# Optimization experiments

Hardware: AMD Instinct MI355X
Metric: run time of the kernel (lower is better)

The kernel has to match this reference:

```python
import jax, jax.numpy as jnp
import numpy as np

B, N, D = 8, 4096, 256
E = 32768
H, C = 4, 64  # heads, per-head dim (hid_dim=256 // heads=4)
NEG_SLOPE = 0.2


def layernorm(x, g, b, eps=1e-5):
    m = jnp.mean(x, axis=-1, keepdims=True)
    v = jnp.var(x, axis=-1, keepdims=True)
    return (x - m) * jax.lax.rsqrt(v + eps) * g + b


def setup_inputs() -> dict:
    key = jax.random.key(0)
    ks = jax.random.split(key, 12)
    def glorot(k, shape):
        lim = np.sqrt(6.0 / (shape[-2] + shape[-1]))
        return jax.random.uniform(k, shape, jnp.float32, -lim, lim)
    return {
        "x": jax.random.normal(ks[0], (B, N, D), jnp.float32),
        "edge_index": jax.random.randint(ks[1], (2, E), 0, N, jnp.int32),
        "W_K": glorot(ks[2], (H * C, D)), "b_K": jnp.zeros((H * C,), jnp.float32),
        "W_V": glorot(ks[3], (H * C, D)), "b_V": jnp.zeros((H * C,), jnp.float32),
        "att_r": glorot(ks[4], (1, H, C)),
        "ln0_g": jnp.ones((H * C,), jnp.float32), "ln0_b": jnp.zeros((H * C,), jnp.float32),
        "ln1_g": jnp.ones((H * C,), jnp.float32), "ln1_b": jnp.zeros((H * C,), jnp.float32),
        "W1": glorot(ks[5], (H * C, H * C)), "b1": jnp.zeros((H * C,), jnp.float32),
        "W2": glorot(ks[6], (H * C, H * C)), "b2": jnp.zeros((H * C,), jnp.float32),
    }


def reference(x, edge_index, W_K, b_K, W_V, b_V, att_r, ln0_g, ln0_b, ln1_g, ln1_b, W1, b1, W2, b2):
    Bq, Nq = x.shape[0], x.shape[1]
    S = Nq  # number of destination segments (fixed for jit)
    src, dst = edge_index[0], edge_index[1]
    # projections -> [B, N, H, C]
    xK = (jnp.einsum('bnd,hd->bnh', x, W_K) + b_K).reshape(Bq, Nq, H, C)
    xV = (jnp.einsum('bnd,hd->bnh', x, W_V) + b_V).reshape(Bq, Nq, H, C)
    # per-node attention logits [B, N, H]
    alpha = jnp.sum(xK * att_r[None], axis=-1)
    # gather to edges, leaky-relu, segment softmax over dst
    a = alpha[:, src]  # [B, E, H]
    a = jnp.where(a >= 0, a, NEG_SLOPE * a)
    a_t = jnp.transpose(a, (1, 0, 2))  # [E, B, H]
    seg_max = jax.ops.segment_max(a_t, dst, num_segments=S)
    seg_max = jnp.where(jnp.isfinite(seg_max), seg_max, 0.0)
    ex = jnp.exp(a_t - seg_max[dst])
    den = jax.ops.segment_sum(ex, dst, num_segments=S)
    w = ex / (den[dst] + 1e-16)  # [E, B, H]
    # weighted scatter-add of values
    v = jnp.transpose(xV[:, src], (1, 0, 2, 3)) * w[..., None]  # [E, B, H, C]
    agg = jax.ops.segment_sum(v, dst, num_segments=S)  # [S, B, H, C]
    out = jnp.transpose(agg, (1, 0, 2, 3)) + att_r[None]  # [B, S, H, C]
    out = out.reshape(Bq, S, H * C)
    out = layernorm(out, ln0_g, ln0_b)
    # rFF: 2-layer MLP, Normalization='None', dropout=0
    h = jax.nn.relu(jnp.einsum('bsd,ed->bse', out, W1) + b1)
    rff = jnp.einsum('bse,fe->bsf', h, W2) + b2
    out = layernorm(out + jax.nn.relu(rff), ln1_g, ln1_b)
    return out
```

## Files before the change

### kernel.cpp

```cpp
#include <hip/hip_runtime.h>
#include <hip/hip_bf16.h>
#include <cstdint>
#include <cstddef>

#define B_   8
#define N_   4096
#define E_   32768
#define ROWS_ 32768
#define NEGSLOPE_ 0.2f
#define NEG_INF_ (-3.402823e38f)

typedef __attribute__((ext_vector_type(8))) __bf16 bf16x8;
typedef __attribute__((ext_vector_type(4))) float  f32x4;

__device__ __forceinline__ float lrelu(float v) { return v >= 0.f ? v : NEGSLOPE_ * v; }

__device__ __forceinline__ float bf2f(ushort u) {
    union { uint32_t i; float f; } c; c.i = ((uint32_t)u) << 16; return c.f;
}
__device__ __forceinline__ ushort f2bf(float f) {
    __hip_bfloat16 h = __float2bfloat16(f);
    return *reinterpret_cast<ushort*>(&h);
}

__device__ __forceinline__ float4 wred_max4(float4 v) {
#pragma unroll
    for (int o = 32; o >= 1; o >>= 1) {
        v.x = fmaxf(v.x, __shfl_xor(v.x, o));
        v.y = fmaxf(v.y, __shfl_xor(v.y, o));
        v.z = fmaxf(v.z, __shfl_xor(v.z, o));
        v.w = fmaxf(v.w, __shfl_xor(v.w, o));
    }
    return v;
}
__device__ __forceinline__ float4 wred_sum4(float4 v) {
#pragma unroll
    for (int o = 32; o >= 1; o >>= 1) {
        v.x += __shfl_xor(v.x, o);
        v.y += __shfl_xor(v.y, o);
        v.z += __shfl_xor(v.z, o);
        v.w += __shfl_xor(v.w, o);
    }
    return v;
}

__global__ void k_prep_u(const float* __restrict__ W_K, const float* __restrict__ b_K,
                         const float* __restrict__ att_r,
                         float* __restrict__ u, float* __restrict__ cvec) {
    int h = blockIdx.x;
    int d = threadIdx.x;
    float s = 0.f;
#pragma unroll 8
    for (int c = 0; c < 64; ++c)
        s += W_K[(size_t)(h*64 + c)*256 + d] * att_r[h*64 + c];
    u[h*256 + d] = s;
    if (d == 0) {
        float cs = 0.f;
        for (int c = 0; c < 64; ++c) cs += b_K[h*64 + c] * att_r[h*64 + c];
        cvec[h] = cs;
    }
}

__global__ void k_cvtW(const float* __restrict__ W_V, const float* __restrict__ W1,
                       const float* __restrict__ W2,
                       ushort* __restrict__ WVb, ushort* __restrict__ W1b,
                       ushort* __restrict__ W2b) {
    int i = blockIdx.x * 1024 + threadIdx.x * 4;
    if (blockIdx.y == 1) {
        int n = i >> 8, c = (i & 255) >> 2;
        const float* s = W1 + (size_t)n*256 + c;
        ushort4 o;
        o.x = f2bf(s[0]);
        o.y = f2bf(s[64]);
        o.z = f2bf(s[128]);
        o.w = f2bf(s[192]);
        *(ushort4*)&W1b[i] = o;
    } else {
        const float* s = (blockIdx.y == 0) ? W_V : W2;
        ushort* d      = (blockIdx.y == 0) ? WVb : W2b;
        float4 v = *(const float4*)&s[i];
        ushort4 o; o.x = f2bf(v.x); o.y = f2bf(v.y); o.z = f2bf(v.z); o.w = f2bf(v.w);
        *(ushort4*)&d[i] = o;
    }
}

__global__ void k_alpha(const float* __restrict__ x, const float* __restrict__ u,
                        const float* __restrict__ cvec, float* __restrict__ alpha,
                        ushort* __restrict__ xb) {
    int wave = threadIdx.x >> 6, lane = threadIdx.x & 63;
    size_t row = (size_t)blockIdx.x * 4 + wave;
    const float4* x4 = (const float4*)(x + row*256);
    float4 xv = x4[lane];
    ushort4 xw; xw.x = f2bf(xv.x); xw.y = f2bf(xv.y); xw.z = f2bf(xv.z); xw.w = f2bf(xv.w);
    *(ushort4*)&xb[row*256 + lane*4] = xw;

    const float4* u4 = (const float4*)u;
    float res[4];
#pragma unroll
    for (int h = 0; h < 4; ++h) {
        float4 uv = u4[h*64 + lane];
        float p = xv.x*uv.x + xv.y*uv.y + xv.z*uv.z + xv.w*uv.w;
#pragma unroll
        for (int o = 32; o >= 1; o >>= 1) p += __shfl_xor(p, o);
        res[h] = p;
    }
    if (lane == 0) {
        float4 cv = *(const float4*)cvec;
        float4 o;
        o.x = lrelu(res[0] + cv.x);
        o.y = lrelu(res[1] + cv.y);
        o.z = lrelu(res[2] + cv.z);
        o.w = lrelu(res[3] + cv.w);
        *(float4*)(alpha + row*4) = o;
    }
}

__global__ void k_hist(const int* __restrict__ ei, int* __restrict__ counts) {
    int e = blockIdx.x * 256 + threadIdx.x;
    if (e < E_) atomicAdd(&counts[ei[E_ + e]], 1);
}

__global__ void k_scan(const int* __restrict__ counts, int* __restrict__ offsets) {
    __shared__ int tot[256];
    int t = threadIdx.x;
    int local[16];
    int s = 0;
#pragma unroll
    for (int i = 0; i < 16; ++i) { local[i] = s; s += counts[t*16 + i]; }
    tot[t] = s;
    __syncthreads();
    for (int d = 1; d < 256; d <<= 1) {
        int v = (t >= d) ? tot[t - d] : 0;
        __syncthreads();
        tot[t] += v;
        __syncthreads();
    }
    int base = (t == 0) ? 0 : tot[t - 1];
#pragma unroll
    for (int i = 0; i < 16; ++i) offsets[t*16 + i] = base + local[i];
    if (t == 255) offsets[4096] = tot[255];
}

__global__ void k_fill(const int* __restrict__ ei, const int* __restrict__ offsets,
                       int* __restrict__ cursor, int* __restrict__ bucket_src) {
    int e = blockIdx.x * 256 + threadIdx.x;
    if (e >= E_) return;
    int d = ei[E_ + e], srcn = ei[e];
    int pos = atomicAdd(&cursor[d], 1);
    bucket_src[offsets[d] + pos] = srcn;
}

__global__ __launch_bounds__(256) void k_agg_ln0(
        const float* __restrict__ alpha, const ushort* __restrict__ xVb,
        const int* __restrict__ offsets, const int* __restrict__ bucket_src,
        const float* __restrict__ att_r,
        const float* __restrict__ g0, const float* __restrict__ b0,
        ushort* __restrict__ out0b) {
    __shared__ float4 s_w4[4][64];
    int t = threadIdx.x, wv = t >> 6, lane = t & 63;
    int gp = blockIdx.x * 4 + wv;
    int n = gp >> 3, b = gp & 7;
    int beg = offsets[n], end = offsets[n + 1];
    size_t brow = (size_t)b * N_;

    float4 m4   = make_float4(NEG_INF_, NEG_INF_, NEG_INF_, NEG_INF_);
    float4 den4 = make_float4(0.f, 0.f, 0.f, 0.f);
    float4 acc4 = make_float4(0.f, 0.f, 0.f, 0.f);

    for (int chunk = beg; chunk < end; chunk += 64) {
        int cnt = min(64, end - chunk);
        int my_src = (lane < cnt) ? bucket_src[chunk + lane] : 0;
        float4 a4 = make_float4(NEG_INF_, NEG_INF_, NEG_INF_, NEG_INF_);
        if (lane < cnt) a4 = *(const float4*)&alpha[(brow + my_src)*4];

        float4 mc = wred_max4(a4);
        float4 mn;
        mn.x = fmaxf(m4.x, mc.x); mn.y = fmaxf(m4.y, mc.y);
        mn.z = fmaxf(m4.z, mc.z); mn.w = fmaxf(m4.w, mc.w);
        float4 ex;
        ex.x = __expf(a4.x - mn.x); ex.y = __expf(a4.y - mn.y);
        ex.z = __expf(a4.z - mn.z); ex.w = __expf(a4.w - mn.w);
        float4 ss = wred_sum4(ex);
        float4 r;
        r.x = __expf(m4.x - mn.x); r.y = __expf(m4.y - mn.y);
        r.z = __expf(m4.z - mn.z); r.w = __expf(m4.w - mn.w);
        den4.x = den4.x * r.x + ss.x; den4.y = den4.y * r.y + ss.y;
        den4.z = den4.z * r.z + ss.z; den4.w = den4.w * r.w + ss.w;
        acc4.x *= r.x; acc4.y *= r.y; acc4.z *= r.z; acc4.w *= r.w;
        m4 = mn;
        s_w4[wv][lane] = ex;

        for (int e = 0; e < cnt; e += 4) {
#pragma unroll
            for (int k = 0; k < 4; ++k) {
                int srcn = __shfl(my_src, e + k);
                float4 w4 = s_w4[wv][e + k];
                ushort4 v = *(const ushort4*)&xVb[(brow + srcn)*256 + lane*4];
                acc4.x += w4.x * bf2f(v.x);
                acc4.y += w4.y * bf2f(v.y);
                acc4.z += w4.z * bf2f(v.z);
                acc4.w += w4.w * bf2f(v.w);
            }
        }
    }

    float4 o4;
    o4.x = acc4.x / (den4.x + 1e-16f) + att_r[lane];
    o4.y = acc4.y / (den4.y + 1e-16f) + att_r[64 + lane];
    o4.z = acc4.z / (den4.z + 1e-16f) + att_r[128 + lane];
    o4.w = acc4.w / (den4.w + 1e-16f) + att_r[192 + lane];

    float s1 = o4.x + o4.y + o4.z + o4.w;
    float s2 = o4.x*o4.x + o4.y*o4.y + o4.z*o4.z + o4.w*o4.w;
#pragma unroll
    for (int o = 32; o >= 1; o >>= 1) { s1 += __shfl_xor(s1, o); s2 += __shfl_xor(s2, o); }
    float mean = s1 * (1.f/256.f);
    float inv = rsqrtf(s2 * (1.f/256.f) - mean*mean + 1e-5f);

    ushort4 st;
    st.x = f2bf((o4.x - mean) * inv * g0[lane]       + b0[lane]);
    st.y = f2bf((o4.y - mean) * inv * g0[64 + lane]  + b0[64 + lane]);
    st.z = f2bf((o4.z - mean) * inv * g0[128 + lane] + b0[128 + lane]);
    st.w = f2bf((o4.w - mean) * inv * g0[192 + lane] + b0[192 + lane]);
    *(ushort4*)&out0b[(brow + n)*256 + lane*4] = st;
}

template<int MODE>
__global__ __launch_bounds__(256) void k_mgemm(const ushort* __restrict__ A,
                                               const ushort* __restrict__ Bw,
                                               const float* __restrict__ bias,
                                               const ushort* __restrict__ res,
                                               const float* __restrict__ g,
                                               const float* __restrict__ bvec,
                                               void* __restrict__ outp) {
    __shared__ __align__(16) ushort As[64*32];
    __shared__ __align__(16) ushort Bs[256*32];
    __shared__ float2 red[64][4];

    int t = threadIdx.x;
    int w = t >> 6, lane = t & 63;
    int fr = lane & 15, fg = lane >> 4;
    size_t m0 = (size_t)blockIdx.x * 64;

    int srow = t >> 2;
    int schunk = (t & 3) ^ (srow & 3);
    const ushort* gA  = A  + (m0 + srow)*256 + schunk*8;
    const ushort* gB0 = Bw + (size_t)srow*256 + schunk*8;

    int chnk = (fg ^ (fr & 3)) * 8;

    f32x4 acc[4][4];
#pragma unroll
    for (int mt = 0; mt < 4; ++mt)
#pragma unroll
        for (int nt = 0; nt < 4; ++nt) acc[mt][nt] = (f32x4){0.f, 0.f, 0.f, 0.f};

    for (int ks = 0; ks < 8; ++ks) {
        int k0 = ks * 32;
        __builtin_amdgcn_global_load_lds(
            (const __attribute__((address_space(1))) void*)(gA + k0),
            (__attribute__((address_space(3))) void*)(&As[t*8]), 16, 0, 0);
#pragma unroll
        for (int rr = 0; rr < 4; ++rr)
            __builtin_amdgcn_global_load_lds(
                (const __attribute__((address_space(1))) void*)(gB0 + rr*16384 + k0),
                (__attribute__((address_space(3))) void*)(&Bs[rr*2048 + t*8]), 16, 0, 0);
        __syncthreads();

        bf16x8 a[4], b[4];
#pragma unroll
        for (int mt = 0; mt < 4; ++mt)
            a[mt] = *(const bf16x8*)&As[(mt*16 + fr)*32 + chnk];
#pragma unroll
        for (int nt = 0; nt < 4; ++nt)
            b[nt] = *(const bf16x8*)&Bs[(w*64 + nt*16 + fr)*32 + chnk];
#pragma unroll
        for (int mt = 0; mt < 4; ++mt)
#pragma unroll
            for (int nt = 0; nt < 4; ++nt)
                acc[mt][nt] = __builtin_amdgcn_mfma_f32_16x16x32_bf16(
                    a[mt], b[nt], acc[mt][nt], 0, 0, 0);
        __syncthreads();
    }

    int colb = w*64 + fr;
    float biasv[4];
#pragma unroll
    for (int nt = 0; nt < 4; ++nt) biasv[nt] = bias[colb + nt*16];

    if (MODE < 2) {
        ushort* ob = (ushort*)outp;
#pragma unroll
        for (int mt = 0; mt < 4; ++mt)
#pragma unroll
            for (int j = 0; j < 4; ++j) {
                int row = mt*16 + fg*4 + j;
#pragma unroll
                for (int nt = 0; nt < 4; ++nt) {
                    float v = acc[mt][nt][j] + biasv[nt];
                    if (MODE == 1) v = fmaxf(v, 0.f);
                    int col = (MODE == 0) ? (((fr + nt*16) << 2) | w)
                                          : (colb + nt*16);
                    ob[(m0 + row)*256 + col] = f2bf(v);
                }
            }
    } else {
        float gv[4], bvv[4];
#pragma unroll
        for (int nt = 0; nt < 4; ++nt) { gv[nt] = g[colb + nt*16]; bvv[nt] = bvec[colb + nt*16]; }
#pragma unroll
        for (int mt = 0; mt < 4; ++mt)
#pragma unroll
            for (int j = 0; j < 4; ++j) {
                int row = mt*16 + fg*4 + j;
                float p1 = 0.f, p2 = 0.f;
#pragma unroll
                for (int nt = 0; nt < 4; ++nt) {
                    float v = acc[mt][nt][j] + biasv[nt];
                    int pc = ((fr + nt*16) << 2) | w;
                    float y = bf2f(res[(m0 + row)*256 + pc]) + fmaxf(v, 0.f);
                    acc[mt][nt][j] = y;
                    p1 += y; p2 += y*y;
                }
#pragma unroll
                for (int o = 8; o >= 1; o >>= 1) { p1 += __shfl_xor(p1, o); p2 += __shfl_xor(p2, o); }
                if (fr == 0) red[row][w] = make_float2(p1, p2);
            }
        __syncthreads();
        float* of = (float*)outp;
#pragma unroll
        for (int mt = 0; mt < 4; ++mt)
#pragma unroll
            for (int j = 0; j < 4; ++j) {
                int row = mt*16 + fg*4 + j;
                float2 s0 = red[row][0], sA = red[row][1], sB = red[row][2], sC = red[row][3];
                float s = s0.x + sA.x + sB.x + sC.x;
                float q = s0.y + sA.y + sB.y + sC.y;
                float mean = s * (1.f/256.f);
                float inv = rsqrtf(q * (1.f/256.f) - mean*mean + 1e-5f);
#pragma unroll
                for (int nt = 0; nt < 4; ++nt)
                    of[(m0 + row)*256 + colb + nt*16] =
                        (acc[mt][nt][j] - mean) * inv * gv[nt] + bvv[nt];
            }
    }
}

extern "C" void kernel_launch(void* const* d_in, const int* in_sizes, int n_in,
                              void* d_out, int out_size, void* d_ws, size_t ws_size,
                              hipStream_t stream) {
    const float* x     = (const float*)d_in[0];
    const int*   ei    = (const int*)  d_in[1];
    const float* W_K   = (const float*)d_in[2];
    const float* b_K   = (const float*)d_in[3];
    const float* W_V   = (const float*)d_in[4];
    const float* b_V   = (const float*)d_in[5];
    const float* att_r = (const float*)d_in[6];
    const float* ln0_g = (const float*)d_in[7];
    const float* ln0_b = (const float*)d_in[8];
    const float* ln1_g = (const float*)d_in[9];
    const float* ln1_b = (const float*)d_in[10];
    const float* W1    = (const float*)d_in[11];
    const float* b1    = (const float*)d_in[12];
    const float* W2    = (const float*)d_in[13];
    const float* b2    = (const float*)d_in[14];
    float* out = (float*)d_out;

    char* wsb = (char*)d_ws;
    float*  u     = (float*) (wsb);
    float*  cvec  = (float*) (wsb + 4096);
    float*  alpha = (float*) (wsb + 8192);
    ushort* WVb   = (ushort*)(wsb + 532480);
    ushort* W1b   = WVb + 65536;
    ushort* W2b   = W1b + 65536;
    int*    ints  = (int*)  (W2b + 65536);
    int* counts   = ints;
    int* cursor   = ints + 4096;
    int* offsets  = ints + 8192;
    int* bucket   = ints + 12544;
    ushort* bufA  = (ushort*)(wsb + 1114112);
    ushort* bufB  = bufA + 8388608;
    size_t need   = 1114112 + 2ull*16777216;

    if (ws_size < need) return;

    hipMemsetAsync(counts, 0, 8192 * sizeof(int), stream);

    k_prep_u <<<4, 256, 0, stream>>>(W_K, b_K, att_r, u, cvec);
    k_cvtW   <<<dim3(64, 3), 256, 0, stream>>>(W_V, W1, W2, WVb, W1b, W2b);
    k_alpha  <<<ROWS_/4, 256, 0, stream>>>(x, u, cvec, alpha, bufA);
    k_mgemm<0><<<ROWS_/64, 256, 0, stream>>>(bufA, WVb, b_V, nullptr, nullptr, nullptr, bufA);
    k_hist   <<<E_/256, 256, 0, stream>>>(ei, counts);
    k_scan   <<<1, 256, 0, stream>>>(counts, offsets);
    k_fill   <<<E_/256, 256, 0, stream>>>(ei, offsets, cursor, bucket);
    k_agg_ln0<<<ROWS_/4, 256, 0, stream>>>(alpha, bufA, offsets, bucket,
                                           att_r, ln0_g, ln0_b, bufB);
    k_mgemm<1><<<ROWS_/64, 256, 0, stream>>>(bufB, W1b, b1, nullptr, nullptr, nullptr, bufA);
    k_mgemm<2><<<ROWS_/64, 256, 0, stream>>>(bufA, W2b, b2, bufB, ln1_g, ln1_b, out);
}
```

Measured before the change: 213.9 us.

## Fuse both MLP GEMMs and the final layernorm into one kernel

Replaces the two separate MLP GEMM launches with a single kernel that keeps the 32-row input tile in LDS, writes the ReLU hidden activations to a swizzled LDS buffer, and runs the second GEMM plus the residual and layernorm from LDS. This removes the hidden-activation round trip through global memory, a second read of the residual, and one launch. In exchange, the tile shrinks from 64 to 32 rows with about 40KB of LDS per block, which lowers occupancy and weight reuse per block, and each block streams both weight matrices.

```diff
diff --git a/kernel.cpp b/kernel.cpp
--- a/kernel.cpp
+++ b/kernel.cpp
@@ -225,17 +225,12 @@
     *(ushort4*)&out0b[(brow + n)*256 + lane*4] = st;
 }
 
-template<int MODE>
-__global__ __launch_bounds__(256) void k_mgemm(const ushort* __restrict__ A,
+__global__ __launch_bounds__(256) void k_gemm0(const ushort* __restrict__ A,
                                                const ushort* __restrict__ Bw,
                                                const float* __restrict__ bias,
-                                               const ushort* __restrict__ res,
-                                               const float* __restrict__ g,
-                                               const float* __restrict__ bvec,
-                                               void* __restrict__ outp) {
+                                               ushort* ob) {
     __shared__ __align__(16) ushort As[64*32];
     __shared__ __align__(16) ushort Bs[256*32];
-    __shared__ float2 red[64][4];
 
     int t = threadIdx.x;
     int w = t >> 6, lane = t & 63;
@@ -283,67 +278,181 @@
         __syncthreads();
     }
 
+    float biasv[4];
+#pragma unroll
+    for (int nt = 0; nt < 4; ++nt) biasv[nt] = bias[w*64 + fr + nt*16];
+#pragma unroll
+    for (int mt = 0; mt < 4; ++mt)
+#pragma unroll
+        for (int j = 0; j < 4; ++j) {
+            int row = mt*16 + fg*4 + j;
+#pragma unroll
+            for (int nt = 0; nt < 4; ++nt) {
+                float v = acc[mt][nt][j] + biasv[nt];
+                int col = ((fr + nt*16) << 2) | w;
+                ob[(m0 + row)*256 + col] = f2bf(v);
+            }
+        }
+}
+
+__global__ __launch_bounds__(256) void k_mlp(const ushort* __restrict__ A,
+                                             const ushort* __restrict__ W1b,
+                                             const float* __restrict__ b1,
+                                             const ushort* __restrict__ W2b,
+                                             const float* __restrict__ b2,
+                                             const float* __restrict__ g,
+                                             const float* __restrict__ bvec,
+                                             float* __restrict__ out) {
+    __shared__ __align__(16) ushort As[8*32*32];
+    __shared__ __align__(16) ushort Bs[256*32];
+    __shared__ __align__(16) ushort Hs[32*256];
+    __shared__ float2 red[32][4];
+
+    int t = threadIdx.x;
+    int w = t >> 6, lane = t & 63;
+    int fr = lane & 15, fg = lane >> 4;
+    size_t m0 = (size_t)blockIdx.x * 32;
+
+    int srow = t >> 2;
+    int schunk = (t & 3) ^ (srow & 3);
+    const ushort* gA  = A   + (m0 + srow)*256 + schunk*8;
+    const ushort* gW1 = W1b + (size_t)srow*256 + schunk*8;
+    const ushort* gW2 = W2b + (size_t)srow*256 + schunk*8;
+
+    int chnk = (fg ^ (fr & 3)) * 8;
+
+    f32x4 acc1[2][4];
+#pragma unroll
+    for (int mt = 0; mt < 2; ++mt)
+#pragma unroll
+        for (int nt = 0; nt < 4; ++nt) acc1[mt][nt] = (f32x4){0.f, 0.f, 0.f, 0.f};
+
+    for (int ks = 0; ks < 8; ++ks) {
+        int k0 = ks * 32;
+        if (t < 128)
+            __builtin_amdgcn_global_load_lds(
+                (const __attribute__((address_space(1))) void*)(gA + k0),
+                (__attribute__((address_space(3))) void*)(&As[ks*1024 + t*8]), 16, 0, 0);
+#pragma unroll
+        for (int rr = 0; rr < 4; ++rr)
+            __builtin_amdgcn_global_load_lds(
+                (const __attribute__((address_space(1))) void*)(gW1 + rr*16384 + k0),
+                (__attribute__((address_space(3))) void*)(&Bs[rr*2048 + t*8]), 16, 0, 0);
+        __syncthreads();
+
+        bf16x8 a[2], b[4];
+#pragma unroll
+        for (int mt = 0; mt < 2; ++mt)
+            a[mt] = *(const bf16x8*)&As[ks*1024 + (mt*16 + fr)*32 + chnk];
+#pragma unroll
+        for (int nt = 0; nt < 4; ++nt)
+            b[nt] = *(const bf16x8*)&Bs[(w*64 + nt*16 + fr)*32 + chnk];
+#pragma unroll
+        for (int mt = 0; mt < 2; ++mt)
+#pragma unroll
+            for (int nt = 0; nt < 4; ++nt)
+                acc1[mt][nt] = __builtin_amdgcn_mfma_f32_16x16x32_bf16(
+                    a[mt], b[nt], acc1[mt][nt], 0, 0, 0);
+        __syncthreads();
+    }
+
     int colb = w*64 + fr;
-    float biasv[4];
-#pragma unroll
-    for (int nt = 0; nt < 4; ++nt) biasv[nt] = bias[colb + nt*16];
-
-    if (MODE < 2) {
-        ushort* ob = (ushort*)outp;
-#pragma unroll
-        for (int mt = 0; mt < 4; ++mt)
+    {
+        float b1v[4];
+#pragma unroll
+        for (int nt = 0; nt < 4; ++nt) b1v[nt] = b1[colb + nt*16];
+#pragma unroll
+        for (int mt = 0; mt < 2; ++mt)
 #pragma unroll
             for (int j = 0; j < 4; ++j) {
                 int row = mt*16 + fg*4 + j;
 #pragma unroll
                 for (int nt = 0; nt < 4; ++nt) {
-                    float v = acc[mt][nt][j] + biasv[nt];
-                    if (MODE == 1) v = fmaxf(v, 0.f);
-                    int col = (MODE == 0) ? (((fr + nt*16) << 2) | w)
-                                          : (colb + nt*16);
-                    ob[(m0 + row)*256 + col] = f2bf(v);
+                    float v = fmaxf(acc1[mt][nt][j] + b1v[nt], 0.f);
+                    int byteoff = (row*512 + (colb + nt*16)*2) ^ ((row & 7) << 4);
+                    *(ushort*)((char*)Hs + byteoff) = f2bf(v);
                 }
             }
-    } else {
-        float gv[4], bvv[4];
-#pragma unroll
-        for (int nt = 0; nt < 4; ++nt) { gv[nt] = g[colb + nt*16]; bvv[nt] = bvec[colb + nt*16]; }
-#pragma unroll
-        for (int mt = 0; mt < 4; ++mt)
-#pragma unroll
-            for (int j = 0; j < 4; ++j) {
-                int row = mt*16 + fg*4 + j;
-                float p1 = 0.f, p2 = 0.f;
-#pragma unroll
-                for (int nt = 0; nt < 4; ++nt) {
-                    float v = acc[mt][nt][j] + biasv[nt];
-                    int pc = ((fr + nt*16) << 2) | w;
-                    float y = bf2f(res[(m0 + row)*256 + pc]) + fmaxf(v, 0.f);
-                    acc[mt][nt][j] = y;
-                    p1 += y; p2 += y*y;
-                }
-#pragma unroll
-                for (int o = 8; o >= 1; o >>= 1) { p1 += __shfl_xor(p1, o); p2 += __shfl_xor(p2, o); }
-                if (fr == 0) red[row][w] = make_float2(p1, p2);
+    }
+    __syncthreads();
+
+    f32x4 acc2[2][4];
+#pragma unroll
+    for (int mt = 0; mt < 2; ++mt)
+#pragma unroll
+        for (int nt = 0; nt < 4; ++nt) acc2[mt][nt] = (f32x4){0.f, 0.f, 0.f, 0.f};
+
+    for (int ks = 0; ks < 8; ++ks) {
+        int k0 = ks * 32;
+#pragma unroll
+        for (int rr = 0; rr < 4; ++rr)
+            __builtin_amdgcn_global_load_lds(
+                (const __attribute__((address_space(1))) void*)(gW2 + rr*16384 + k0),
+                (__attribute__((address_space(3))) void*)(&Bs[rr*2048 + t*8]), 16, 0, 0);
+        __syncthreads();
+
+        bf16x8 a[2], b[4];
+#pragma unroll
+        for (int mt = 0; mt < 2; ++mt) {
+            int row = mt*16 + fr;
+            int byteoff = (row*512 + (k0 + fg*8)*2) ^ ((row & 7) << 4);
+            a[mt] = *(const bf16x8*)((char*)Hs + byteoff);
+        }
+#pragma unroll
+        for (int nt = 0; nt < 4; ++nt)
+            b[nt] = *(const bf16x8*)&Bs[(w*64 + nt*16 + fr)*32 + chnk];
+#pragma unroll
+        for (int mt = 0; mt < 2; ++mt)
+#pragma unroll
+            for (int nt = 0; nt < 4; ++nt)
+                acc2[mt][nt] = __builtin_amdgcn_mfma_f32_16x16x32_bf16(
+                    a[mt], b[nt], acc2[mt][nt], 0, 0, 0);
+        __syncthreads();
+    }
+
+    float b2v[4], gv[4], bvv[4];
+#pragma unroll
+    for (int nt = 0; nt < 4; ++nt) {
+        b2v[nt] = b2[colb + nt*16];
+        gv[nt]  = g[colb + nt*16];
+        bvv[nt] = bvec[colb + nt*16];
+    }
+#pragma unroll
+    for (int mt = 0; mt < 2; ++mt)
+#pragma unroll
+        for (int j = 0; j < 4; ++j) {
+            int row = mt*16 + fg*4 + j;
+            float p1 = 0.f, p2 = 0.f;
+#pragma unroll
+            for (int nt = 0; nt < 4; ++nt) {
+                float v = fmaxf(acc2[mt][nt][j] + b2v[nt], 0.f);
+                int kp  = ((nt*16 + fr) << 2) | w;
+                int ks2 = kp >> 5, off = kp & 31;
+                int idx = ks2*1024 + row*32 + ((off >> 3) ^ (row & 3))*8 + (off & 7);
+                float y = bf2f(As[idx]) + v;
+                acc2[mt][nt][j] = y;
+                p1 += y; p2 += y*y;
             }
-        __syncthreads();
-        float* of = (float*)outp;
-#pragma unroll
-        for (int mt = 0; mt < 4; ++mt)
-#pragma unroll
-            for (int j = 0; j < 4; ++j) {
-                int row = mt*16 + fg*4 + j;
-                float2 s0 = red[row][0], sA = red[row][1], sB = red[row][2], sC = red[row][3];
-                float s = s0.x + sA.x + sB.x + sC.x;
-                float q = s0.y + sA.y + sB.y + sC.y;
-                float mean = s * (1.f/256.f);
-                float inv = rsqrtf(q * (1.f/256.f) - mean*mean + 1e-5f);
-#pragma unroll
-                for (int nt = 0; nt < 4; ++nt)
-                    of[(m0 + row)*256 + colb + nt*16] =
-                        (acc[mt][nt][j] - mean) * inv * gv[nt] + bvv[nt];
-            }
-    }
+#pragma unroll
+            for (int o = 8; o >= 1; o >>= 1) { p1 += __shfl_xor(p1, o); p2 += __shfl_xor(p2, o); }
+            if (fr == 0) red[row][w] = make_float2(p1, p2);
+        }
+    __syncthreads();
+#pragma unroll
+    for (int mt = 0; mt < 2; ++mt)
+#pragma unroll
+        for (int j = 0; j < 4; ++j) {
+            int row = mt*16 + fg*4 + j;
+            float2 s0 = red[row][0], sA = red[row][1], sB = red[row][2], sC = red[row][3];
+            float s = s0.x + sA.x + sB.x + sC.x;
+            float q = s0.y + sA.y + sB.y + sC.y;
+            float mean = s * (1.f/256.f);
+            float inv = rsqrtf(q * (1.f/256.f) - mean*mean + 1e-5f);
+#pragma unroll
+            for (int nt = 0; nt < 4; ++nt)
+                out[(m0 + row)*256 + colb + nt*16] =
+                    (acc2[mt][nt][j] - mean) * inv * gv[nt] + bvv[nt];
+        }
 }
 
 extern "C" void kernel_launch(void* const* d_in, const int* in_sizes, int n_in,
@@ -389,12 +498,12 @@
     k_prep_u <<<4, 256, 0, stream>>>(W_K, b_K, att_r, u, cvec);
     k_cvtW   <<<dim3(64, 3), 256, 0, stream>>>(W_V, W1, W2, WVb, W1b, W2b);
     k_alpha  <<<ROWS_/4, 256, 0, stream>>>(x, u, cvec, alpha, bufA);
-    k_mgemm<0><<<ROWS_/64, 256, 0, stream>>>(bufA, WVb, b_V, nullptr, nullptr, nullptr, bufA);
+    k_gemm0  <<<ROWS_/64, 256, 0, stream>>>(bufA, WVb, b_V, bufA);
     k_hist   <<<E_/256, 256, 0, stream>>>(ei, counts);
     k_scan   <<<1, 256, 0, stream>>>(counts, offsets);
     k_fill   <<<E_/256, 256, 0, stream>>>(ei, offsets, cursor, bucket);
     k_agg_ln0<<<ROWS_/4, 256, 0, stream>>>(alpha, bufA, offsets, bucket,
                                            att_r, ln0_g, ln0_b, bufB);
-    k_mgemm<1><<<ROWS_/64, 256, 0, stream>>>(bufB, W1b, b1, nullptr, nullptr, nullptr, bufA);
-    k_mgemm<2><<<ROWS_/64, 256, 0, stream>>>(bufA, W2b, b2, bufB, ln1_g, ln1_b, out);
-}
+    k_mlp    <<<ROWS_/32, 256, 0, stream>>>(bufB, W1b, b1, W2b, b2,
+                                            ln1_g, ln1_b, out);
+}
```

Measured after the change: 209.0 us. 2.3% less time.
